# Kernel tuning notes

Hardware: AMD Instinct MI355X
Metric: run time of the kernel (lower is better)

The kernel has to match this reference:

```python
import jax, jax.numpy as jnp
import numpy as np

MB, C, H, W = 128, 2048, 8, 4  # h*w must equal 32 (hard-coded repeat(1,32,1,1))
DG, DF, DOUT = 256, 256, 128


def setup_inputs() -> dict:
    key = jax.random.key(0)
    ks = jax.random.split(key, 15)
    s = 0.02
    return {
        "x": jax.random.normal(ks[0], (MB, 1, C, H, W), dtype=jnp.float32),
        "Wg1": jax.random.normal(ks[1], (2 * C, DG), dtype=jnp.float32) * s,
        "bg1": jnp.zeros((DG,), jnp.float32),
        "Wg2": jax.random.normal(ks[2], (DG, DG), dtype=jnp.float32) * s,
        "bg2": jnp.zeros((DG,), jnp.float32),
        "Wg3": jax.random.normal(ks[3], (DG, DG), dtype=jnp.float32) * s,
        "bg3": jnp.zeros((DG,), jnp.float32),
        "Wg4": jax.random.normal(ks[4], (DG, DG), dtype=jnp.float32) * s,
        "bg4": jnp.zeros((DG,), jnp.float32),
        "Wf1": jax.random.normal(ks[5], (DG, DF), dtype=jnp.float32) * s,
        "bf1": jnp.zeros((DF,), jnp.float32),
        "Wfc2": jax.random.normal(ks[6], (DF, DF), dtype=jnp.float32) * s,
        "bfc2": jnp.zeros((DF,), jnp.float32),
        "Wfc3": jax.random.normal(ks[7], (DF, DOUT), dtype=jnp.float32) * s,
        "bfc3": jnp.zeros((DOUT,), jnp.float32),
    }


def reference(x, Wg1, bg1, Wg2, bg2, Wg3, bg3, Wg4, bg4, Wf1, bf1, Wfc2, bfc2, Wfc3, bfc3):
    x = x[:, 0]  # squeeze(dim=1) -> [mb, C, h, w]
    mb, c, h, w = x.shape
    p = h * w  # 32 spatial positions
    x_flat = x.reshape(mb, c, p).transpose(0, 2, 1)  # [mb, p, C]
    # g_fc1 on cat([x_i, x_j]): split the weight instead of materializing
    # the [mb, p, p, 2C] concat tensor. cat last-dim = [x_flat[b,i], x_flat[b,j]]
    # where i varies over dim 2 and j over dim 1.
    W1a, W1b = Wg1[:c], Wg1[c:]
    A = jnp.einsum('bpc,cd->bpd', x_flat, W1a)  # contribution of x_i
    B = jnp.einsum('bpc,cd->bpd', x_flat, W1b)  # contribution of x_j
    hp = jax.nn.relu(A[:, None, :, :] + B[:, :, None, :] + bg1)  # [mb,p,p,256]
    hp = jax.nn.relu(hp @ Wg2 + bg2)
    hp = jax.nn.relu(hp @ Wg3 + bg3)
    hp = jax.nn.relu(hp @ Wg4 + bg4)
    x_g = hp.sum(axis=(1, 2))  # sum over all p*p pairs -> [mb, 256]
    x_f = jax.nn.relu(x_g @ Wf1 + bf1)
    y = jax.nn.relu(x_f @ Wfc2 + bfc2)  # fcout.fc2 + relu (dropout treated as eval/identity)
    return y @ Wfc3 + bfc3  # [mb, 128]
```

## Files before the change

kernel.cpp:

```cpp
#include <hip/hip_runtime.h>
#include <hip/hip_bf16.h>
#include <stdint.h>

using short8  = __attribute__((ext_vector_type(8))) short;
using f32x4   = __attribute__((ext_vector_type(4))) float;
using f32x16  = __attribute__((ext_vector_type(16))) float;
using uint4v  = __attribute__((ext_vector_type(4))) unsigned int;

#define MFMA16(a,b,c) __builtin_amdgcn_mfma_f32_16x16x32_bf16((a),(b),(c),0,0,0)
#define MFMA32(a,b,c) __builtin_amdgcn_mfma_f32_32x32x16_bf16((a),(b),(c),0,0,0)
#define SWZ15(row, byteoff) ((byteoff) ^ (((row)&15)<<4))

__device__ inline short f2bf(float f){
  unsigned u = __float_as_uint(f);
  u += 0x7fff + ((u>>16)&1);
  return (short)(u>>16);
}
__device__ inline unsigned pack2(float a, float b){
  return __builtin_amdgcn_perm(__float_as_uint(b) + 0x8000u,
                               __float_as_uint(a) + 0x8000u, 0x07060302u);
}

__global__ __launch_bounds__(256) void k_prep(const float* __restrict__ x,
                                              short* __restrict__ xfrag,
                                              const float* __restrict__ Wg1,
                                              const float* __restrict__ Wg2,
                                              const float* __restrict__ Wg3,
                                              const float* __restrict__ Wg4,
                                              short* __restrict__ w1f,
                                              short* __restrict__ w2f,
                                              short* __restrict__ w3f,
                                              short* __restrict__ w4f){
  __shared__ float tile[256][33];
  const int bid = blockIdx.x, t = threadIdx.x;
  if (bid < 1024){
    const int ck = bid & 7, b = bid >> 3;
    const float* xb = x + (size_t)b*2048*32 + (size_t)ck*256*32;
#pragma unroll
    for (int r = 0; r < 32; r++){
      int idx = r*256 + t;
      tile[idx>>5][idx&31] = xb[idx];
    }
    __syncthreads();
    short* ob = xfrag + (size_t)(b*8 + ck)*8192;
#pragma unroll
    for (int i4 = 0; i4 < 4; i4++){
      int s = i4*256 + t;
      int mt = s>>9, kk = (s>>6)&7, l = s&63;
      int tok = mt*16 + (l&15);
      int cb = kk*32 + (l>>4)*8;
      short8 o;
#pragma unroll
      for (int j = 0; j < 8; j++) o[j] = f2bf(tile[cb+j][tok]);
      *(short8*)(ob + (size_t)s*8) = o;
    }
  } else {
    int g = (bid - 1024)*256 + t;
    if (g < 32*64*64){
      int l = g & 63, kk = (g>>6) & 63, ct = g>>12;
      int d = ct*16 + (l&15);
      int cbase = kk*32 + (l>>4)*8;
      short* o = w1f + (size_t)g*8;
#pragma unroll
      for (int i = 0; i < 8; i++){
        int c = cbase + i;
        float v = (d < 256) ? Wg1[(size_t)c*256 + d]
                            : Wg1[(size_t)(2048 + c)*256 + (d - 256)];
        o[i] = f2bf(v);
      }
    } else {
      int g2 = g - 32*64*64;
      int L = g2 / 8192;
      int r = g2 - L*8192;
      int l = r & 63, kk = (r>>6)&15, ct = r>>10;
      const float* W = (L==0) ? Wg2 : (L==1) ? Wg3 : Wg4;
      short* o = ((L==0) ? w2f : (L==1) ? w3f : w4f) + (size_t)r*8;
      int d = ct*32 + (l&31);
      int k0 = kk*16 + (l>>5)*8;
#pragma unroll
      for (int i = 0; i < 8; i++) o[i] = f2bf(W[(size_t)(k0+i)*256 + d]);
    }
  }
}

__global__ __launch_bounds__(128) void k_ab(const short* __restrict__ xfrag,
                                            const short* __restrict__ w1f,
                                            float* __restrict__ AB){
  const int wid = threadIdx.x>>6, l = threadIdx.x&63;
  const int b = blockIdx.x;
  const int ctb = blockIdx.y*4 + wid*2;
  const int hi = l>>4, lo16 = l&15;
  f32x4 acc[2][2] = {};
  const short* xb = xfrag + (size_t)b*65536 + (size_t)l*8;
  const short* wb = w1f + (size_t)l*8;
#pragma unroll 1
  for (int ck = 0; ck < 8; ck++){
#pragma unroll
    for (int kk = 0; kk < 8; kk++){
      short8 af0 = *(const short8*)(xb + (size_t)ck*8192 + kk*512);
      short8 af1 = *(const short8*)(xb + (size_t)ck*8192 + 4096 + kk*512);
      short8 wf0 = *(const short8*)(wb + ((size_t)(ctb  )*64 + ck*8 + kk)*512);
      short8 wf1 = *(const short8*)(wb + ((size_t)(ctb+1)*64 + ck*8 + kk)*512);
      acc[0][0] = MFMA16(wf0, af0, acc[0][0]);
      acc[1][0] = MFMA16(wf0, af1, acc[1][0]);
      acc[0][1] = MFMA16(wf1, af0, acc[0][1]);
      acc[1][1] = MFMA16(wf1, af1, acc[1][1]);
    }
  }
#pragma unroll
  for (int mt = 0; mt < 2; mt++){
    int m = b*32 + mt*16 + lo16;
#pragma unroll
    for (int dt = 0; dt < 2; dt++){
      int d0 = (ctb+dt)*16 + hi*4;
      *(f32x4*)(AB + (size_t)m*512 + d0) = acc[mt][dt];
    }
  }
}

__global__ __launch_bounds__(512) void k_heavy(const float* __restrict__ AB,
                                               const short* __restrict__ w2f,
                                               const short* __restrict__ w3f,
                                               const short* __restrict__ w4f,
                                               const float* __restrict__ bg1,
                                               const float* __restrict__ bg2,
                                               const float* __restrict__ bg3,
                                               const float* __restrict__ bg4,
                                               float* __restrict__ xgp){
  __shared__ short act[128*256];
  const int b = blockIdx.y, qg = blockIdx.x, t = threadIdx.x;
  char* abase = (char*)act;

#pragma unroll
  for (int it = 0; it < 8; it++){
    int ch = it*512 + t;
    int m = ch>>5, c0 = (ch&31)*8;
    int q = qg*4 + (m>>5), p = m&31;
    const float* Ap = AB + (size_t)(b*32+p)*512 + c0;
    const float* Bp = AB + (size_t)(b*32+q)*512 + 256 + c0;
    f32x4 a0 = *(const f32x4*)Ap,       a1 = *(const f32x4*)(Ap+4);
    f32x4 b0 = *(const f32x4*)Bp,       b1 = *(const f32x4*)(Bp+4);
    f32x4 g0 = *(const f32x4*)(bg1+c0), g1 = *(const f32x4*)(bg1+c0+4);
    uint4v w;
    w[0] = pack2(fmaxf(a0[0]+b0[0]+g0[0],0.f), fmaxf(a0[1]+b0[1]+g0[1],0.f));
    w[1] = pack2(fmaxf(a0[2]+b0[2]+g0[2],0.f), fmaxf(a0[3]+b0[3]+g0[3],0.f));
    w[2] = pack2(fmaxf(a1[0]+b1[0]+g1[0],0.f), fmaxf(a1[1]+b1[1]+g1[1],0.f));
    w[3] = pack2(fmaxf(a1[2]+b1[2]+g1[2],0.f), fmaxf(a1[3]+b1[3]+g1[3],0.f));
    *(uint4v*)(abase + SWZ15(m, m*512 + c0*2)) = w;
  }
  __syncthreads();

  const int w = t>>6, l = t&63;
  const int tok = l&31, hi = l>>5;
  const short* wfr[3]  = {w2f, w3f, w4f};
  const float* bias[3] = {bg2, bg3, bg4};

#pragma unroll
  for (int L = 0; L < 3; L++){
    const short* wp = wfr[L] + ((size_t)(w*16)*64 + l)*8;
    f32x16 acc[4];
#pragma unroll
    for (int gq = 0; gq < 4; gq++){
      f32x4 bb = *(const f32x4*)(bias[L] + w*32 + gq*8 + hi*4);
#pragma unroll
      for (int j = 0; j < 4; j++){
        float v = bb[j];
#pragma unroll
        for (int mt = 0; mt < 4; mt++) acc[mt][gq*4+j] = v;
      }
    }
#pragma unroll
    for (int kk = 0; kk < 16; kk++){
      short8 wf = *(const short8*)(wp + (size_t)kk*512);
      short8 af[4];
#pragma unroll
      for (int mt = 0; mt < 4; mt++){
        int m = mt*32 + tok;
        af[mt] = *(const short8*)(abase + SWZ15(m, m*512 + kk*32 + hi*16));
      }
#pragma unroll
      for (int mt = 0; mt < 4; mt++)
        acc[mt] = MFMA32(wf, af[mt], acc[mt]);
    }

    if (L < 2){
      __syncthreads();
#pragma unroll
      for (int mt = 0; mt < 4; mt++){
        int m = mt*32 + tok;
#pragma unroll
        for (int gq = 0; gq < 4; gq++){
          int d0 = w*32 + gq*8 + hi*4;
          unsigned lo2 = pack2(fmaxf(acc[mt][gq*4+0],0.f), fmaxf(acc[mt][gq*4+1],0.f));
          unsigned hi2 = pack2(fmaxf(acc[mt][gq*4+2],0.f), fmaxf(acc[mt][gq*4+3],0.f));
          *(uint2*)(abase + SWZ15(m, m*512 + d0*2)) = make_uint2(lo2, hi2);
        }
      }
      __syncthreads();
    } else {
#pragma unroll
      for (int gq = 0; gq < 4; gq++){
        int d0 = w*32 + gq*8 + hi*4;
        f32x4 s;
#pragma unroll
        for (int j = 0; j < 4; j++){
          float v = fmaxf(acc[0][gq*4+j],0.f) + fmaxf(acc[1][gq*4+j],0.f)
                  + fmaxf(acc[2][gq*4+j],0.f) + fmaxf(acc[3][gq*4+j],0.f);
          s[j] = v;
        }
#pragma unroll
        for (int off = 1; off < 32; off <<= 1){
          s[0] += __shfl_xor(s[0], off);
          s[1] += __shfl_xor(s[1], off);
          s[2] += __shfl_xor(s[2], off);
          s[3] += __shfl_xor(s[3], off);
        }
        if (tok == 0)
          *(f32x4*)(xgp + ((size_t)b*8 + qg)*256 + d0) = s;
      }
    }
  }
}

__global__ __launch_bounds__(512) void k_final(const float* __restrict__ xgp,
                                               const float* __restrict__ Wf1,
                                               const float* __restrict__ bf1,
                                               const float* __restrict__ Wfc2,
                                               const float* __restrict__ bfc2,
                                               const float* __restrict__ Wfc3,
                                               const float* __restrict__ bfc3,
                                               float* __restrict__ out){
  __shared__ float b0[256], b1[256], b2[256], part[2][256], part3[4][128];
  const int b = blockIdx.x, t = threadIdx.x;
  if (t < 256){
    float s = 0.f;
#pragma unroll
    for (int g = 0; g < 8; g++) s += xgp[((size_t)b*8 + g)*256 + t];
    b0[t] = s;
  }
  __syncthreads();
  const int d = t & 255, cg = t >> 8;
  {
    float a = cg ? 0.f : bf1[d];
#pragma unroll 8
    for (int c = cg*128; c < cg*128 + 128; c++) a += b0[c] * Wf1[c*256 + d];
    part[cg][d] = a;
  }
  __syncthreads();
  if (t < 256) b1[t] = fmaxf(part[0][t] + part[1][t], 0.f);
  __syncthreads();
  {
    float a = cg ? 0.f : bfc2[d];
#pragma unroll 8
    for (int c = cg*128; c < cg*128 + 128; c++) a += b1[c] * Wfc2[c*256 + d];
    part[cg][d] = a;
  }
  __syncthreads();
  if (t < 256) b2[t] = fmaxf(part[0][t] + part[1][t], 0.f);
  __syncthreads();
  {
    const int d3 = t & 127, cg3 = t >> 7;
    float o = cg3 ? 0.f : bfc3[d3];
#pragma unroll 8
    for (int c = cg3*64; c < cg3*64 + 64; c++) o += b2[c] * Wfc3[c*128 + d3];
    part3[cg3][d3] = o;
  }
  __syncthreads();
  if (t < 128)
    out[(size_t)b*128 + t] = part3[0][t] + part3[1][t] + part3[2][t] + part3[3][t];
}

extern "C" void kernel_launch(void* const* d_in, const int* in_sizes, int n_in,
                              void* d_out, int out_size, void* d_ws, size_t ws_size,
                              hipStream_t stream){
  const float* x    = (const float*)d_in[0];
  const float* Wg1  = (const float*)d_in[1];
  const float* bg1  = (const float*)d_in[2];
  const float* Wg2  = (const float*)d_in[3];
  const float* bg2  = (const float*)d_in[4];
  const float* Wg3  = (const float*)d_in[5];
  const float* bg3  = (const float*)d_in[6];
  const float* Wg4  = (const float*)d_in[7];
  const float* bg4  = (const float*)d_in[8];
  const float* Wf1  = (const float*)d_in[9];
  const float* bf1  = (const float*)d_in[10];
  const float* Wfc2 = (const float*)d_in[11];
  const float* bfc2 = (const float*)d_in[12];
  const float* Wfc3 = (const float*)d_in[13];
  const float* bfc3 = (const float*)d_in[14];
  float* out = (float*)d_out;

  char* ws = (char*)d_ws;
  short* xfrag = (short*)(ws);
  short* w1f   = (short*)(ws + 16777216);
  short* w2f   = (short*)(ws + 18874368);
  short* w3f   = (short*)(ws + 19005440);
  short* w4f   = (short*)(ws + 19136512);
  float* AB    = (float*)(ws + 19267584);
  float* xgp   = (float*)(ws + 16777216);

  k_prep<<<1632, 256, 0, stream>>>(x, xfrag, Wg1, Wg2, Wg3, Wg4, w1f, w2f, w3f, w4f);
  k_ab<<<dim3(128,8), 128, 0, stream>>>(xfrag, w1f, AB);
  k_heavy<<<dim3(8,128), 512, 0, stream>>>(AB, w2f, w3f, w4f, bg1, bg2, bg3, bg4, xgp);
  k_final<<<128, 512, 0, stream>>>(xgp, Wf1, bf1, Wfc2, bfc2, Wfc3, bfc3, out);
}
```

Before: 115.6 us.

## Keep pair activations in registers and stage layer weights in LDS

The heavy MLP kernel is restructured so each wave owns one q row (32 pairs) and keeps its activations in MFMA B-fragment registers across all three layers. Lane-swap shuffles re-pack outputs into inputs, replacing the round trip through an LDS activation buffer. The LDS is repurposed to hold 6 of the 8 column tiles of each layer's weights, and the other 2 tiles are read from global memory. The grid changes to 128x4 blocks, each covering 8 q values, with a block-level partial sum, so k_final now reduces 4 partials instead of 8. This cuts LDS activation traffic and barriers but adds register pressure (8 f32x16 accumulators plus 16 fragments) and some uncached global weight reads.

```diff
diff --git a/kernel.cpp b/kernel.cpp
--- a/kernel.cpp
+++ b/kernel.cpp
@@ -9,7 +9,6 @@
 
 #define MFMA16(a,b,c) __builtin_amdgcn_mfma_f32_16x16x32_bf16((a),(b),(c),0,0,0)
 #define MFMA32(a,b,c) __builtin_amdgcn_mfma_f32_32x32x16_bf16((a),(b),(c),0,0,0)
-#define SWZ15(row, byteoff) ((byteoff) ^ (((row)&15)<<4))
 
 __device__ inline short f2bf(float f){
   unsigned u = __float_as_uint(f);
@@ -19,6 +18,11 @@
 __device__ inline unsigned pack2(float a, float b){
   return __builtin_amdgcn_perm(__float_as_uint(b) + 0x8000u,
                                __float_as_uint(a) + 0x8000u, 0x07060302u);
+}
+
+union FragU { uint4v u; short8 s; };
+__device__ inline short8 mk8(unsigned w0, unsigned w1, unsigned w2, unsigned w3){
+  FragU f; f.u = (uint4v){w0, w1, w2, w3}; return f.s;
 }
 
 __global__ __launch_bounds__(256) void k_prep(const float* __restrict__ x,
@@ -118,7 +122,7 @@
   }
 }
 
-__global__ __launch_bounds__(512) void k_heavy(const float* __restrict__ AB,
+__global__ __launch_bounds__(512, 2) void k_heavy(const float* __restrict__ AB,
                                                const short* __restrict__ w2f,
                                                const short* __restrict__ w3f,
                                                const short* __restrict__ w4f,
@@ -127,96 +131,141 @@
                                                const float* __restrict__ bg3,
                                                const float* __restrict__ bg4,
                                                float* __restrict__ xgp){
-  __shared__ short act[128*256];
-  const int b = blockIdx.y, qg = blockIdx.x, t = threadIdx.x;
-  char* abase = (char*)act;
-
-#pragma unroll
-  for (int it = 0; it < 8; it++){
-    int ch = it*512 + t;
-    int m = ch>>5, c0 = (ch&31)*8;
-    int q = qg*4 + (m>>5), p = m&31;
-    const float* Ap = AB + (size_t)(b*32+p)*512 + c0;
-    const float* Bp = AB + (size_t)(b*32+q)*512 + 256 + c0;
-    f32x4 a0 = *(const f32x4*)Ap,       a1 = *(const f32x4*)(Ap+4);
-    f32x4 b0 = *(const f32x4*)Bp,       b1 = *(const f32x4*)(Bp+4);
-    f32x4 g0 = *(const f32x4*)(bg1+c0), g1 = *(const f32x4*)(bg1+c0+4);
-    uint4v w;
-    w[0] = pack2(fmaxf(a0[0]+b0[0]+g0[0],0.f), fmaxf(a0[1]+b0[1]+g0[1],0.f));
-    w[1] = pack2(fmaxf(a0[2]+b0[2]+g0[2],0.f), fmaxf(a0[3]+b0[3]+g0[3],0.f));
-    w[2] = pack2(fmaxf(a1[0]+b1[0]+g1[0],0.f), fmaxf(a1[1]+b1[1]+g1[1],0.f));
-    w[3] = pack2(fmaxf(a1[2]+b1[2]+g1[2],0.f), fmaxf(a1[3]+b1[3]+g1[3],0.f));
-    *(uint4v*)(abase + SWZ15(m, m*512 + c0*2)) = w;
-  }
-  __syncthreads();
-
-  const int w = t>>6, l = t&63;
-  const int tok = l&31, hi = l>>5;
+  __shared__ short wlds[49152];
+  __shared__ float part[8][256];
+  const int b = blockIdx.x, qg8 = blockIdx.y, t = threadIdx.x;
+  const int w = t>>6, l = t&63, tok = l&31, hi = l>>5;
+  const int q = qg8*8 + w;
+
+  {
+    const char* src = (const char*)w2f;
+    char* dst = (char*)wlds;
+#pragma unroll
+    for (int i = 0; i < 12; i++){
+      int off = (i*512 + t)*16;
+      *(uint4v*)(dst + off) = *(const uint4v*)(src + off);
+    }
+  }
+
+  short8 frag[16];
+  {
+    const float* Ap = AB + ((size_t)(b*32) + tok)*512;
+    const float* Bq = AB + ((size_t)(b*32) + q)*512 + 256;
+#pragma unroll
+    for (int kk = 0; kk < 16; kk++){
+      int k0 = kk*16 + hi*8;
+      f32x4 a0 = *(const f32x4*)(Ap + k0), a1 = *(const f32x4*)(Ap + k0 + 4);
+      f32x4 q0 = *(const f32x4*)(Bq + k0), q1 = *(const f32x4*)(Bq + k0 + 4);
+      f32x4 g0 = *(const f32x4*)(bg1 + k0), g1 = *(const f32x4*)(bg1 + k0 + 4);
+      unsigned w0 = pack2(fmaxf(a0[0]+q0[0]+g0[0],0.f), fmaxf(a0[1]+q0[1]+g0[1],0.f));
+      unsigned w1 = pack2(fmaxf(a0[2]+q0[2]+g0[2],0.f), fmaxf(a0[3]+q0[3]+g0[3],0.f));
+      unsigned w2 = pack2(fmaxf(a1[0]+q1[0]+g1[0],0.f), fmaxf(a1[1]+q1[1]+g1[1],0.f));
+      unsigned w3 = pack2(fmaxf(a1[2]+q1[2]+g1[2],0.f), fmaxf(a1[3]+q1[3]+g1[3],0.f));
+      frag[kk] = mk8(w0, w1, w2, w3);
+    }
+  }
+  __syncthreads();
+
   const short* wfr[3]  = {w2f, w3f, w4f};
   const float* bias[3] = {bg2, bg3, bg4};
 
 #pragma unroll
   for (int L = 0; L < 3; L++){
-    const short* wp = wfr[L] + ((size_t)(w*16)*64 + l)*8;
-    f32x16 acc[4];
-#pragma unroll
-    for (int gq = 0; gq < 4; gq++){
-      f32x4 bb = *(const f32x4*)(bias[L] + w*32 + gq*8 + hi*4);
-#pragma unroll
-      for (int j = 0; j < 4; j++){
-        float v = bb[j];
-#pragma unroll
-        for (int mt = 0; mt < 4; mt++) acc[mt][gq*4+j] = v;
-      }
-    }
-#pragma unroll
-    for (int kk = 0; kk < 16; kk++){
-      short8 wf = *(const short8*)(wp + (size_t)kk*512);
-      short8 af[4];
-#pragma unroll
-      for (int mt = 0; mt < 4; mt++){
-        int m = mt*32 + tok;
-        af[mt] = *(const short8*)(abase + SWZ15(m, m*512 + kk*32 + hi*16));
-      }
-#pragma unroll
-      for (int mt = 0; mt < 4; mt++)
-        acc[mt] = MFMA32(wf, af[mt], acc[mt]);
+    f32x16 acc[8];
+#pragma unroll
+    for (int ct = 0; ct < 8; ct++)
+#pragma unroll
+      for (int r = 0; r < 16; r++) acc[ct][r] = 0.f;
+
+#pragma unroll
+    for (int ct = 0; ct < 8; ct++){
+#pragma unroll
+      for (int kk = 0; kk < 16; kk++){
+        short8 wf;
+        if (ct < 6)
+          wf = *(const short8*)((const char*)wlds + (((ct*16 + kk)*64 + l) << 4));
+        else
+          wf = *(const short8*)(wfr[L] + ((size_t)((ct*16 + kk)*64 + l))*8);
+        acc[ct] = MFMA32(wf, frag[kk], acc[ct]);
+      }
     }
 
     if (L < 2){
       __syncthreads();
-#pragma unroll
-      for (int mt = 0; mt < 4; mt++){
-        int m = mt*32 + tok;
-#pragma unroll
-        for (int gq = 0; gq < 4; gq++){
-          int d0 = w*32 + gq*8 + hi*4;
-          unsigned lo2 = pack2(fmaxf(acc[mt][gq*4+0],0.f), fmaxf(acc[mt][gq*4+1],0.f));
-          unsigned hi2 = pack2(fmaxf(acc[mt][gq*4+2],0.f), fmaxf(acc[mt][gq*4+3],0.f));
-          *(uint2*)(abase + SWZ15(m, m*512 + d0*2)) = make_uint2(lo2, hi2);
+      {
+        const char* src = (const char*)wfr[L+1];
+        char* dst = (char*)wlds;
+#pragma unroll
+        for (int i = 0; i < 12; i++){
+          int off = (i*512 + t)*16;
+          *(uint4v*)(dst + off) = *(const uint4v*)(src + off);
         }
+      }
+#pragma unroll
+      for (int ct = 0; ct < 8; ct++){
+        const float* bp = bias[L] + ct*32 + hi*4;
+        f32x4 b0v = *(const f32x4*)(bp);
+        f32x4 b1v = *(const f32x4*)(bp + 8);
+        f32x4 b2v = *(const f32x4*)(bp + 16);
+        f32x4 b3v = *(const f32x4*)(bp + 24);
+        float t0  = fmaxf(acc[ct][ 0] + b0v[0], 0.f);
+        float t1  = fmaxf(acc[ct][ 1] + b0v[1], 0.f);
+        float t2  = fmaxf(acc[ct][ 2] + b0v[2], 0.f);
+        float t3  = fmaxf(acc[ct][ 3] + b0v[3], 0.f);
+        float t4  = fmaxf(acc[ct][ 4] + b1v[0], 0.f);
+        float t5  = fmaxf(acc[ct][ 5] + b1v[1], 0.f);
+        float t6  = fmaxf(acc[ct][ 6] + b1v[2], 0.f);
+        float t7  = fmaxf(acc[ct][ 7] + b1v[3], 0.f);
+        float t8  = fmaxf(acc[ct][ 8] + b2v[0], 0.f);
+        float t9  = fmaxf(acc[ct][ 9] + b2v[1], 0.f);
+        float t10 = fmaxf(acc[ct][10] + b2v[2], 0.f);
+        float t11 = fmaxf(acc[ct][11] + b2v[3], 0.f);
+        float t12 = fmaxf(acc[ct][12] + b3v[0], 0.f);
+        float t13 = fmaxf(acc[ct][13] + b3v[1], 0.f);
+        float t14 = fmaxf(acc[ct][14] + b3v[2], 0.f);
+        float t15 = fmaxf(acc[ct][15] + b3v[3], 0.f);
+        unsigned u0 = pack2(t0,t1),   u1 = pack2(t2,t3);
+        unsigned v0 = pack2(t4,t5),   v1 = pack2(t6,t7);
+        unsigned x0 = pack2(t8,t9),   x1 = pack2(t10,t11);
+        unsigned y0 = pack2(t12,t13), y1 = pack2(t14,t15);
+        unsigned eu0 = __shfl_xor(u0, 32), eu1 = __shfl_xor(u1, 32);
+        unsigned ev0 = __shfl_xor(v0, 32), ev1 = __shfl_xor(v1, 32);
+        unsigned ex0 = __shfl_xor(x0, 32), ex1 = __shfl_xor(x1, 32);
+        unsigned ey0 = __shfl_xor(y0, 32), ey1 = __shfl_xor(y1, 32);
+        frag[ct*2    ] = mk8(hi ? ev0 : u0,  hi ? ev1 : u1,
+                             hi ? v0  : eu0, hi ? v1  : eu1);
+        frag[ct*2 + 1] = mk8(hi ? ey0 : x0,  hi ? ey1 : x1,
+                             hi ? y0  : ex0, hi ? y1  : ex1);
       }
       __syncthreads();
     } else {
 #pragma unroll
-      for (int gq = 0; gq < 4; gq++){
-        int d0 = w*32 + gq*8 + hi*4;
-        f32x4 s;
-#pragma unroll
-        for (int j = 0; j < 4; j++){
-          float v = fmaxf(acc[0][gq*4+j],0.f) + fmaxf(acc[1][gq*4+j],0.f)
-                  + fmaxf(acc[2][gq*4+j],0.f) + fmaxf(acc[3][gq*4+j],0.f);
-          s[j] = v;
+      for (int ct = 0; ct < 8; ct++){
+        const float* bp = bias[2] + ct*32 + hi*4;
+#pragma unroll
+        for (int gq = 0; gq < 4; gq++){
+          f32x4 bb = *(const f32x4*)(bp + gq*8);
+          f32x4 s;
+#pragma unroll
+          for (int j = 0; j < 4; j++)
+            s[j] = fmaxf(acc[ct][gq*4 + j] + bb[j], 0.f);
+#pragma unroll
+          for (int off = 1; off < 32; off <<= 1){
+            s[0] += __shfl_xor(s[0], off);
+            s[1] += __shfl_xor(s[1], off);
+            s[2] += __shfl_xor(s[2], off);
+            s[3] += __shfl_xor(s[3], off);
+          }
+          if (tok == 0)
+            *(f32x4*)(&part[w][ct*32 + gq*8 + hi*4]) = s;
         }
-#pragma unroll
-        for (int off = 1; off < 32; off <<= 1){
-          s[0] += __shfl_xor(s[0], off);
-          s[1] += __shfl_xor(s[1], off);
-          s[2] += __shfl_xor(s[2], off);
-          s[3] += __shfl_xor(s[3], off);
-        }
-        if (tok == 0)
-          *(f32x4*)(xgp + ((size_t)b*8 + qg)*256 + d0) = s;
+      }
+      __syncthreads();
+      if (t < 256){
+        float s = 0.f;
+#pragma unroll
+        for (int ww = 0; ww < 8; ww++) s += part[ww][t];
+        xgp[((size_t)b*4 + qg8)*256 + t] = s;
       }
     }
   }
@@ -235,7 +284,7 @@
   if (t < 256){
     float s = 0.f;
 #pragma unroll
-    for (int g = 0; g < 8; g++) s += xgp[((size_t)b*8 + g)*256 + t];
+    for (int g = 0; g < 4; g++) s += xgp[((size_t)b*4 + g)*256 + t];
     b0[t] = s;
   }
   __syncthreads();
@@ -301,6 +350,6 @@
 
   k_prep<<<1632, 256, 0, stream>>>(x, xfrag, Wg1, Wg2, Wg3, Wg4, w1f, w2f, w3f, w4f);
   k_ab<<<dim3(128,8), 128, 0, stream>>>(xfrag, w1f, AB);
-  k_heavy<<<dim3(8,128), 512, 0, stream>>>(AB, w2f, w3f, w4f, bg1, bg2, bg3, bg4, xgp);
+  k_heavy<<<dim3(128,4), 512, 0, stream>>>(AB, w2f, w3f, w4f, bg1, bg2, bg3, bg4, xgp);
   k_final<<<128, 512, 0, stream>>>(xgp, Wf1, bf1, Wfc2, bfc2, Wfc3, bfc3, out);
 }
```

New measurement: 181.0 us. 56.5% more time.
